# Kernel optimization log

Hardware: AMD Instinct MI355X
Metric: run time of the kernel (lower is better)

The kernel has to match this reference:

```python
import jax, jax.numpy as jnp
import numpy as np

N_NODES = 100000
N_EDGES = 1600000
IN_DIM = 128
HID_DIM = 128
N_MASK = 5000
N_CLASSES = 4


def gcn_layer(x, src, dst, edge_weight, W, b):
    """PyG GCNConv: x' = D^{-1/2} (A + I) D^{-1/2} (x W) + b, with edge weights."""
    n = x.shape[0]
    loop = jnp.arange(n, dtype=src.dtype)
    s = jnp.concatenate([src, loop])                      # [E+N]
    d = jnp.concatenate([dst, loop])                      # [E+N]
    w = jnp.concatenate([edge_weight, jnp.ones((n,), edge_weight.dtype)])
    deg = jax.ops.segment_sum(w, d, num_segments=n)       # weighted in-degree incl. self-loop
    dis = jnp.where(deg > 0, jax.lax.rsqrt(deg), 0.0)     # deg^{-1/2}, inf -> 0
    norm = dis[s] * w * dis[d]                            # [E+N]
    h = x @ W                                             # [N, H] small GEMM
    msg = h[s] * norm[:, None]                            # gather + scale  [E+N, H]
    out = jax.ops.segment_sum(msg, d, num_segments=n)     # scatter-add     [N, H]
    return out + b


def setup_inputs() -> dict:
    key = jax.random.key(0)
    ks = jax.random.split(key, 8)
    x = jax.random.normal(ks[0], (N_NODES, IN_DIM), dtype=jnp.float32)
    edge_weight = jax.random.uniform(ks[1], (N_EDGES,), dtype=jnp.float32)
    W1 = jax.random.normal(ks[2], (IN_DIM, HID_DIM), dtype=jnp.float32) * (1.0 / np.sqrt(IN_DIM))
    b1 = jnp.zeros((HID_DIM,), jnp.float32)
    W2 = jax.random.normal(ks[3], (HID_DIM, HID_DIM), dtype=jnp.float32) * (1.0 / np.sqrt(HID_DIM))
    b2 = jnp.zeros((HID_DIM,), jnp.float32)
    edge_index = jax.random.randint(ks[4], (2, N_EDGES), 0, N_NODES, dtype=jnp.int32)
    mask_idx = jax.random.randint(ks[5], (N_MASK,), 0, N_NODES, dtype=jnp.int32)
    y = jax.random.randint(ks[6], (N_NODES,), 0, N_CLASSES, dtype=jnp.int32)
    return {"x": x, "edge_weight": edge_weight, "W1": W1, "b1": b1,
            "W2": W2, "b2": b2, "edge_index": edge_index,
            "mask_idx": mask_idx, "y": y}


def reference(x, edge_weight, W1, b1, W2, b2, edge_index, mask_idx, y):
    src, dst = edge_index[0], edge_index[1]
    h = gcn_layer(x, src, dst, edge_weight, W1, b1)
    h = jax.nn.relu(h)
    # F.dropout(training=False) in eval mode is identity
    h = gcn_layer(h, src, dst, edge_weight, W2, b2)
    return h[mask_idx], y[mask_idx]
```

## Files before the change

kernel.cpp:

```cpp
#include <hip/hip_runtime.h>

constexpr int N = 100000;
constexpr int E = 1600000;
constexpr int D = 128;
constexpr int M = 5000;

constexpr int MF_BLKS = (N + 255) / 256;

constexpr int NB  = 196;
constexpr int EB  = 2048;
constexpr int NPB = (E + EB - 1) / EB;
constexpr int HL  = NB * NPB;
constexpr int SC_BLKS = (HL + 1023) / 1024;
constexpr int PREP_BLKS = 64;
constexpr int MB_BLKS = (M + 255) / 256;

typedef __attribute__((ext_vector_type(8))) short bf16x8;
typedef __attribute__((ext_vector_type(4))) float f32x4;


__device__ __forceinline__ unsigned int pack_bf16x2(float a, float b) {
    unsigned int ua = __float_as_uint(a);
    unsigned int ub = __float_as_uint(b);
    ua = (ua + 0x7FFFu + ((ua >> 16) & 1u)) >> 16;
    ub = (ub + 0x7FFFu + ((ub >> 16) & 1u)) & 0xFFFF0000u;
    return ua | ub;
}
__device__ __forceinline__ unsigned short bf16_rne(float a) {
    unsigned int ua = __float_as_uint(a);
    return (unsigned short)((ua + 0x7FFFu + ((ua >> 16) & 1u)) >> 16);
}
__device__ __forceinline__ float bf16_lo(unsigned int u) { return __uint_as_float(u << 16); }
__device__ __forceinline__ float bf16_hi(unsigned int u) { return __uint_as_float(u & 0xFFFF0000u); }


__global__ __launch_bounds__(256) void k_misc1(const int* __restrict__ dst,
                                               int* __restrict__ hist,
                                               const float* __restrict__ W1,
                                               unsigned int* __restrict__ Wt1,
                                               const float* __restrict__ W2,
                                               unsigned int* __restrict__ Wt2,
                                               const int* __restrict__ mask,
                                               unsigned int* __restrict__ maskbit,
                                               unsigned int* __restrict__ needed) {
    __shared__ int h[NB];
    const int t = threadIdx.x;
    if (blockIdx.x < NPB) {
        if (t < NB) h[t] = 0;
        __syncthreads();
        const int base = blockIdx.x * EB;
#pragma unroll
        for (int i = 0; i < 8; ++i) {
            int e = base + t + i * 256;
            if (e < E) {
                int b = __builtin_nontemporal_load(dst + e) >> 9;
                atomicAdd(&h[b], 1);
            }
        }
        __syncthreads();
        if (t < NB) hist[t * NPB + blockIdx.x] = h[t];
    } else if (blockIdx.x < NPB + PREP_BLKS) {
        int gi = (blockIdx.x - NPB) * 256 + t;
        const float* W = (gi < 8192) ? W1 : W2;
        unsigned int* Wt = (gi < 8192) ? Wt1 : Wt2;
        int idx = gi & 8191;
        int n = idx >> 6, kk = idx & 63;
        float a = W[(2 * kk) * D + n];
        float b = W[(2 * kk + 1) * D + n];
        Wt[idx] = pack_bf16x2(a, b);
    } else {
        int i = (blockIdx.x - NPB - PREP_BLKS) * 256 + t;
        if (i < M) {
            int n = mask[i];
            atomicOr(&maskbit[n >> 5], 1u << (n & 31));
            atomicOr(&needed[n >> 5], 1u << (n & 31));
        }
    }
}


__global__ __launch_bounds__(256) void k_misc2(const int* __restrict__ hist,
                                               int* __restrict__ bs,
                                               const unsigned int* __restrict__ maskbit,
                                               const int* __restrict__ src,
                                               const int* __restrict__ dst,
                                               unsigned int* __restrict__ needed) {
    __shared__ int ws_[4];
    const int t = threadIdx.x;
    if (blockIdx.x < SC_BLKS) {
        const int idx = blockIdx.x * 1024 + t * 4;
        int s = 0;
        if (idx + 3 < HL) {
            int4 c = *(const int4*)(hist + idx);
            s = c.x + c.y + c.z + c.w;
        } else {
            for (int i = 0; i < 4; ++i) if (idx + i < HL) s += hist[idx + i];
        }
        for (int off = 32; off > 0; off >>= 1) s += __shfl_down(s, off);
        if ((t & 63) == 0) ws_[t >> 6] = s;
        __syncthreads();
        if (t == 0) bs[blockIdx.x] = ws_[0] + ws_[1] + ws_[2] + ws_[3];
    } else {
        const int base = (blockIdx.x - SC_BLKS) * EB;
#pragma unroll
        for (int i = 0; i < 8; ++i) {
            int e = base + t + i * 256;
            if (e < E) {
                int d = __builtin_nontemporal_load(dst + e);
                if ((maskbit[d >> 5] >> (d & 31)) & 1u) {
                    int s = src[e];
                    atomicOr(&needed[s >> 5], 1u << (s & 31));
                }
            }
        }
    }
}


__global__ __launch_bounds__(256) void k_scanf(const int* __restrict__ hist,
                                               const int* __restrict__ bs,
                                               int* __restrict__ histS) {
    __shared__ int sh[256];
    __shared__ int waveS[4];
    const int t = threadIdx.x;
    const int lane = t & 63;
    const int wave = t >> 6;

    sh[t] = (t < SC_BLKS) ? bs[t] : 0;
    __syncthreads();
    for (int off = 1; off < 256; off <<= 1) {
        int u = (t >= off) ? sh[t - off] : 0;
        __syncthreads();
        sh[t] += u;
        __syncthreads();
    }
    const int bOff = sh[blockIdx.x] - bs[blockIdx.x];

    const int idx = blockIdx.x * 1024 + t * 4;
    int4 c = make_int4(0, 0, 0, 0);
    if (idx + 3 < HL) c = *(const int4*)(hist + idx);
    else {
        if (idx + 0 < HL) c.x = hist[idx + 0];
        if (idx + 1 < HL) c.y = hist[idx + 1];
        if (idx + 2 < HL) c.z = hist[idx + 2];
        if (idx + 3 < HL) c.w = hist[idx + 3];
    }
    int s = c.x + c.y + c.z + c.w;

    int v = s;
    for (int off = 1; off < 64; off <<= 1) {
        int u = __shfl_up(v, off);
        if (lane >= off) v += u;
    }
    if (lane == 63) waveS[wave] = v;
    __syncthreads();
    int waveBase = 0;
    for (int w = 0; w < 4; ++w) if (w < wave) waveBase += waveS[w];
    int excl = bOff + waveBase + (v - s);

    int4 rs;
    rs.x = excl;
    rs.y = excl + c.x;
    rs.z = excl + c.x + c.y;
    rs.w = excl + c.x + c.y + c.z;
    if (idx + 3 < HL) {
        *(int4*)(histS + idx) = rs;
    } else {
        if (idx + 0 < HL) histS[idx + 0] = rs.x;
        if (idx + 1 < HL) histS[idx + 1] = rs.y;
        if (idx + 2 < HL) histS[idx + 2] = rs.z;
        if (idx + 3 < HL) histS[idx + 3] = rs.w;
    }
}


template <bool BF16IN>
__device__ __forceinline__ void gemm_mfma_body(const void* __restrict__ Xin,
                                               const unsigned int* __restrict__ Wt,
                                               unsigned short* __restrict__ out, int blk) {
    __shared__ unsigned int Ws[128 * 68];
    const int t = threadIdx.x;
#pragma unroll
    for (int i = 0; i < 8; ++i) {
        int f4 = t + i * 256;
        int n = f4 >> 4;
        int k4 = f4 & 15;
        uint4 w = ((const uint4*)Wt)[f4];
        *(uint4*)(&Ws[n * 68 + k4 * 4]) = w;
    }
    __syncthreads();

    const int wv = t >> 6, lane = t & 63;
    const int q = lane >> 4, l15 = lane & 15;
    const int rowBase = blk * 256 + wv * 64;

    f32x4 acc[4][8] = {};
#pragma unroll
    for (int kc = 0; kc < 4; ++kc) {
        bf16x8 af[4];
#pragma unroll
        for (int rt = 0; rt < 4; ++rt) {
            int row = rowBase + rt * 16 + l15;
            if (row > N - 1) row = N - 1;
            union { uint4 u; bf16x8 v; } cv;
            if (BF16IN) {
                cv.u = *(const uint4*)((const unsigned int*)Xin + (size_t)row * 64 + kc * 16 + q * 4);
            } else {
                const float* xr = (const float*)Xin + (size_t)row * D + kc * 32 + q * 8;
                float4 x0 = *(const float4*)xr;
                float4 x1 = *(const float4*)(xr + 4);
                cv.u.x = pack_bf16x2(x0.x, x0.y);
                cv.u.y = pack_bf16x2(x0.z, x0.w);
                cv.u.z = pack_bf16x2(x1.x, x1.y);
                cv.u.w = pack_bf16x2(x1.z, x1.w);
            }
            af[rt] = cv.v;
        }
#pragma unroll
        for (int ct = 0; ct < 8; ++ct) {
            union { uint4 u; bf16x8 v; } bv;
            bv.u = *(const uint4*)(&Ws[(ct * 16 + l15) * 68 + kc * 16 + q * 4]);
#pragma unroll
            for (int rt = 0; rt < 4; ++rt)
                acc[rt][ct] = __builtin_amdgcn_mfma_f32_16x16x32_bf16(af[rt], bv.v, acc[rt][ct], 0, 0, 0);
        }
    }

#pragma unroll
    for (int rt = 0; rt < 4; ++rt) {
#pragma unroll
        for (int ct = 0; ct < 8; ++ct) {
            int col = ct * 16 + l15;
#pragma unroll
            for (int r = 0; r < 4; ++r) {
                int row = rowBase + rt * 16 + q * 4 + r;
                if (row < N) out[(size_t)row * D + col] = bf16_rne(acc[rt][ct][r]);
            }
        }
    }
}


__global__ __launch_bounds__(256) void k_part_g1(const int* __restrict__ src,
                                                 const int* __restrict__ dst,
                                                 const float* __restrict__ ew,
                                                 const int* __restrict__ histS,
                                                 unsigned long long* __restrict__ tmp,
                                                 const float* __restrict__ x,
                                                 const unsigned int* __restrict__ Wt1,
                                                 unsigned short* __restrict__ A) {
    if (blockIdx.x >= NPB) {
        gemm_mfma_body<false>(x, Wt1, A, blockIdx.x - NPB);
        return;
    }
    __shared__ int base_[NB];
    const int t = threadIdx.x;
    if (t < NB) base_[t] = histS[t * NPB + blockIdx.x];
    __syncthreads();
    const int eb = blockIdx.x * EB;
#pragma unroll
    for (int i = 0; i < 8; ++i) {
        int e = eb + t + i * 256;
        if (e < E) {
            int d = __builtin_nontemporal_load(dst + e);
            int s = __builtin_nontemporal_load(src + e);
            float w = __builtin_nontemporal_load(ew + e);
            int b = d >> 9;
            int pos = atomicAdd(&base_[b], 1);
            unsigned long long rec =
                ((unsigned long long)(unsigned int)__float_as_int(w) << 32) |
                ((unsigned int)s << 9) | (unsigned int)(d & 511);
            __builtin_nontemporal_store(rec, tmp + pos);
        }
    }
}

__global__ __launch_bounds__(256) void k_gemm2(const unsigned short* __restrict__ B,
                                               const unsigned int* __restrict__ Wt2,
                                               unsigned short* __restrict__ A2) {
    gemm_mfma_body<true>(B, Wt2, A2, blockIdx.x);
}


__global__ __launch_bounds__(256) void k_local(const unsigned long long* __restrict__ tmp,
                                               const int* __restrict__ histS,
                                               float* __restrict__ dis,
                                               int* __restrict__ rowStart,
                                               int2* __restrict__ pairs) {
    const int b = blockIdx.x;
    const int t = threadIdx.x;
    const int segBeg = histS[b * NPB];
    const int segEnd = (b + 1 < NB) ? histS[(b + 1) * NPB] : E;

    __shared__ int   cnt[512];
    __shared__ float wsum[512];
    __shared__ int   off[512];
    __shared__ int   waveS[4];
    cnt[t] = 0; cnt[t + 256] = 0;
    wsum[t] = 0.f; wsum[t + 256] = 0.f;
    __syncthreads();

    for (int e = segBeg + t; e < segEnd; e += 256) {
        unsigned long long rec = tmp[e];
        int dl = (int)(rec & 511);
        float w = __uint_as_float((unsigned int)(rec >> 32));
        atomicAdd(&cnt[dl], 1);
        atomicAdd(&wsum[dl], w);
    }
    __syncthreads();

    const int i0 = t * 2, i1 = t * 2 + 1;
    const int c0 = cnt[i0], c1 = cnt[i1];
    const int pv = c0 + c1;
    const int lane = t & 63, wv = t >> 6;
    int v = pv;
    for (int o = 1; o < 64; o <<= 1) {
        int u = __shfl_up(v, o);
        if (lane >= o) v += u;
    }
    if (lane == 63) waveS[wv] = v;
    __syncthreads();
    int wb = 0;
    for (int w = 0; w < 4; ++w) if (w < wv) wb += waveS[w];
    const int ex = wb + v - pv;
    off[i0] = ex;
    off[i1] = ex + c0;
    const int node0 = b * 512 + i0, node1 = b * 512 + i1;
    if (node0 < N) { rowStart[node0] = segBeg + ex;      dis[node0] = rsqrtf(1.0f + wsum[i0]); }
    if (node1 < N) { rowStart[node1] = segBeg + ex + c0; dis[node1] = rsqrtf(1.0f + wsum[i1]); }
    cnt[i0] = 0; cnt[i1] = 0;
    if (b == NB - 1 && t == 0) rowStart[N] = E;
    __syncthreads();

    for (int e = segBeg + t; e < segEnd; e += 256) {
        unsigned long long rec = tmp[e];
        int dl = (int)(rec & 511);
        int s  = (int)((rec >> 9) & 0xFFFFF);
        unsigned int wbits = (unsigned int)(rec >> 32);
        int r = atomicAdd(&cnt[dl], 1);
        pairs[segBeg + off[dl] + r] = make_int2(s, (int)wbits);
    }
}


__global__ __launch_bounds__(256) void k_aggregate(const unsigned int* __restrict__ Hb,
                                                   const int2* __restrict__ pairs,
                                                   const int* __restrict__ rowStart,
                                                   const float* __restrict__ dis,
                                                   const unsigned int* __restrict__ needed,
                                                   const float* __restrict__ b,
                                                   unsigned int* __restrict__ outB) {
    int node = blockIdx.x * 4 + (threadIdx.x >> 6);
    if (node >= N) return;
    if (!((needed[node >> 5] >> (node & 31)) & 1u)) return;
    int lane = threadIdx.x & 63;
    int beg = rowStart[node], end = rowStart[node + 1];

    float ax = 0.f, ay = 0.f;
    int j = beg;
    for (; j + 7 < end; j += 8) {
        int2 p[8];
        float vv[8];
        unsigned int h[8];
#pragma unroll
        for (int i = 0; i < 8; ++i) p[i] = pairs[j + i];
#pragma unroll
        for (int i = 0; i < 8; ++i) { h[i] = Hb[(size_t)p[i].x * 64 + lane]; vv[i] = dis[p[i].x]; }
#pragma unroll
        for (int i = 0; i < 8; ++i) {
            float v = __int_as_float(p[i].y) * vv[i];
            ax += bf16_lo(h[i]) * v;
            ay += bf16_hi(h[i]) * v;
        }
    }
    for (; j + 3 < end; j += 4) {
        int2 p[4];
        float vv[4];
        unsigned int h[4];
#pragma unroll
        for (int i = 0; i < 4; ++i) p[i] = pairs[j + i];
#pragma unroll
        for (int i = 0; i < 4; ++i) { h[i] = Hb[(size_t)p[i].x * 64 + lane]; vv[i] = dis[p[i].x]; }
#pragma unroll
        for (int i = 0; i < 4; ++i) {
            float v = __int_as_float(p[i].y) * vv[i];
            ax += bf16_lo(h[i]) * v;
            ay += bf16_hi(h[i]) * v;
        }
    }
    for (; j < end; ++j) {
        int2 p0 = pairs[j];
        unsigned int h0 = Hb[(size_t)p0.x * 64 + lane];
        float v0 = __int_as_float(p0.y) * dis[p0.x];
        ax += bf16_lo(h0) * v0;
        ay += bf16_hi(h0) * v0;
    }

    float dd = dis[node];
    float sn = dd * dd;
    unsigned int hs = Hb[(size_t)node * 64 + lane];
    float2 bb = ((const float2*)b)[lane];
    float ox = fmaxf(ax * dd + bf16_lo(hs) * sn + bb.x, 0.f);
    float oy = fmaxf(ay * dd + bf16_hi(hs) * sn + bb.y, 0.f);
    __builtin_nontemporal_store(pack_bf16x2(ox, oy), outB + (size_t)node * 64 + lane);
}


__global__ __launch_bounds__(256) void k_aggregate_mask(const unsigned int* __restrict__ Hb,
                                                        const int2* __restrict__ pairs,
                                                        const int* __restrict__ rowStart,
                                                        const float* __restrict__ dis,
                                                        const float* __restrict__ b,
                                                        const int* __restrict__ mask,
                                                        const int* __restrict__ y,
                                                        float* __restrict__ out) {
    int i = blockIdx.x * 4 + (threadIdx.x >> 6);
    if (i >= M) return;
    int lane = threadIdx.x & 63;
    int node = mask[i];
    int beg = rowStart[node], end = rowStart[node + 1];

    float ax = 0.f, ay = 0.f;
    int j = beg;
    for (; j + 7 < end; j += 8) {
        int2 p[8];
        float vv[8];
        unsigned int h[8];
#pragma unroll
        for (int ii = 0; ii < 8; ++ii) p[ii] = pairs[j + ii];
#pragma unroll
        for (int ii = 0; ii < 8; ++ii) { h[ii] = Hb[(size_t)p[ii].x * 64 + lane]; vv[ii] = dis[p[ii].x]; }
#pragma unroll
        for (int ii = 0; ii < 8; ++ii) {
            float v = __int_as_float(p[ii].y) * vv[ii];
            ax += bf16_lo(h[ii]) * v;
            ay += bf16_hi(h[ii]) * v;
        }
    }
    for (; j < end; ++j) {
        int2 p0 = pairs[j];
        unsigned int h0 = Hb[(size_t)p0.x * 64 + lane];
        float v0 = __int_as_float(p0.y) * dis[p0.x];
        ax += bf16_lo(h0) * v0;
        ay += bf16_hi(h0) * v0;
    }

    float dd = dis[node];
    float sn = dd * dd;
    unsigned int hs = Hb[(size_t)node * 64 + lane];
    float2 bb = ((const float2*)b)[lane];
    float ox = ax * dd + bf16_lo(hs) * sn + bb.x;
    float oy = ay * dd + bf16_hi(hs) * sn + bb.y;
    ((float2*)(out + (size_t)i * D))[lane] = make_float2(ox, oy);
    if (lane == 0) out[(size_t)M * D + i] = (float)y[node];
}

extern "C" void kernel_launch(void* const* d_in, const int* in_sizes, int n_in,
                              void* d_out, int out_size, void* d_ws, size_t ws_size,
                              hipStream_t stream) {
    const float* x  = (const float*)d_in[0];
    const float* ew = (const float*)d_in[1];
    const float* W1 = (const float*)d_in[2];
    const float* b1 = (const float*)d_in[3];
    const float* W2 = (const float*)d_in[4];
    const float* b2 = (const float*)d_in[5];
    const int* eidx = (const int*)d_in[6];
    const int* mask = (const int*)d_in[7];
    const int* y    = (const int*)d_in[8];
    const int* src = eidx;
    const int* dst = eidx + E;

    char* ws = (char*)d_ws;
    float* dis      = (float*)(ws);
    int*   rowStart = (int*)(ws + (size_t)512 * 1024);
    int*   scanBS   = (int*)(ws + (size_t)1024 * 1024);
    unsigned int* maskbit = (unsigned int*)(ws + (size_t)1056 * 1024);
    unsigned int* needed  = (unsigned int*)(ws + (size_t)1072 * 1024);
    unsigned int* Wt1 = (unsigned int*)(ws + (size_t)1088 * 1024);
    unsigned int* Wt2 = (unsigned int*)(ws + (size_t)1120 * 1024);
    int*   hist     = (int*)(ws + (size_t)1280 * 1024);
    int*   histS    = (int*)(ws + (size_t)1920 * 1024);
    int2*  pairs    = (int2*)(ws + (size_t)3 * 1024 * 1024);
    unsigned long long* tmp = (unsigned long long*)(ws + (size_t)16 * 1024 * 1024);
    unsigned short* A  = (unsigned short*)(ws + (size_t)29 * 1024 * 1024);
    unsigned short* B  = (unsigned short*)(ws + (size_t)55 * 1024 * 1024);
    unsigned short* A2 = (unsigned short*)(ws + (size_t)81 * 1024 * 1024);

    (void)hipMemsetAsync(maskbit, 0, (size_t)32 * 1024, stream);
    hipLaunchKernelGGL(k_misc1, dim3(NPB + PREP_BLKS + MB_BLKS), dim3(256), 0, stream,
                       dst, hist, W1, Wt1, W2, Wt2, mask, maskbit, needed);

    hipLaunchKernelGGL(k_misc2, dim3(SC_BLKS + NPB), dim3(256), 0, stream,
                       hist, scanBS, maskbit, src, dst, needed);
    hipLaunchKernelGGL(k_scanf, dim3(SC_BLKS), dim3(256), 0, stream, hist, scanBS, histS);

    hipLaunchKernelGGL(k_part_g1, dim3(NPB + MF_BLKS), dim3(256), 0, stream,
                       src, dst, ew, histS, tmp, x, Wt1, A);
    hipLaunchKernelGGL(k_local, dim3(NB), dim3(256), 0, stream, tmp, histS, dis, rowStart, pairs);

    hipLaunchKernelGGL(k_aggregate, dim3((N + 3) / 4), dim3(256), 0, stream,
                       (const unsigned int*)A, pairs, rowStart, dis, needed, b1,
                       (unsigned int*)B);

    hipLaunchKernelGGL(k_gemm2, dim3(MF_BLKS), dim3(256), 0, stream, B, Wt2, A2);
    hipLaunchKernelGGL(k_aggregate_mask, dim3((M + 3) / 4), dim3(256), 0, stream,
                       (const unsigned int*)A2, pairs, rowStart, dis, b2, mask, y, (float*)d_out);
}
```

Before: 290.0 us.

## Fuse CSR-build kernels into one cooperative kernel with grid syncs

```diff
diff --git a/kernel.cpp b/kernel.cpp
--- a/kernel.cpp
+++ b/kernel.cpp
@@ -1,4 +1,7 @@
 #include <hip/hip_runtime.h>
+#include <hip/hip_cooperative_groups.h>
+
+namespace cg = cooperative_groups;
 
 constexpr int N = 100000;
 constexpr int E = 1600000;
@@ -15,6 +18,13 @@
 constexpr int PREP_BLKS = 64;
 constexpr int MB_BLKS = (M + 255) / 256;
 
+constexpr int CSR_GRID = 768;
+constexpr int S0_UNITS = 2 + NPB + PREP_BLKS;
+constexpr int S1_UNITS = MB_BLKS + SC_BLKS;
+constexpr int S2_UNITS = NPB + SC_BLKS;
+constexpr int S3_UNITS = NPB;
+constexpr int S4_UNITS = NB;
+
 typedef __attribute__((ext_vector_type(8))) short bf16x8;
 typedef __attribute__((ext_vector_type(4))) float f32x4;
 
@@ -34,142 +44,231 @@
 __device__ __forceinline__ float bf16_hi(unsigned int u) { return __uint_as_float(u & 0xFFFF0000u); }
 
 
-__global__ __launch_bounds__(256) void k_misc1(const int* __restrict__ dst,
-                                               int* __restrict__ hist,
-                                               const float* __restrict__ W1,
-                                               unsigned int* __restrict__ Wt1,
-                                               const float* __restrict__ W2,
-                                               unsigned int* __restrict__ Wt2,
-                                               const int* __restrict__ mask,
-                                               unsigned int* __restrict__ maskbit,
-                                               unsigned int* __restrict__ needed) {
-    __shared__ int h[NB];
+__global__ __launch_bounds__(256) void k_csr(const int* __restrict__ src,
+                                             const int* __restrict__ dst,
+                                             const float* __restrict__ ew,
+                                             const int* __restrict__ mask,
+                                             const float* __restrict__ W1,
+                                             const float* __restrict__ W2,
+                                             int* __restrict__ hist,
+                                             int* __restrict__ bs,
+                                             int* __restrict__ histS,
+                                             unsigned long long* __restrict__ tmp,
+                                             int2* __restrict__ pairs,
+                                             float* __restrict__ dis,
+                                             int* __restrict__ rowStart,
+                                             unsigned int* __restrict__ maskbit,
+                                             unsigned int* __restrict__ needed,
+                                             unsigned int* __restrict__ Wt1,
+                                             unsigned int* __restrict__ Wt2) {
+    cg::grid_group grid = cg::this_grid();
     const int t = threadIdx.x;
-    if (blockIdx.x < NPB) {
-        if (t < NB) h[t] = 0;
-        __syncthreads();
-        const int base = blockIdx.x * EB;
+    const int nb = gridDim.x;
+
+    __shared__ int   h[NB];
+    __shared__ int   sh[256];
+    __shared__ int   waveS[4];
+    __shared__ int   cnt[512];
+    __shared__ float wsum[512];
+    __shared__ int   off[512];
+
+    for (int u = blockIdx.x; u < S0_UNITS; u += nb) {
+        if (u < 2) {
+            unsigned int* p = (u == 0) ? maskbit : needed;
+            for (int i = t; i < 4096; i += 256) p[i] = 0u;
+        } else if (u < 2 + NPB) {
+            const int ub = u - 2;
+            if (t < NB) h[t] = 0;
+            __syncthreads();
+            const int base = ub * EB;
+#pragma unroll
+            for (int i = 0; i < 8; ++i) {
+                int e = base + t + i * 256;
+                if (e < E) {
+                    int b = __builtin_nontemporal_load(dst + e) >> 9;
+                    atomicAdd(&h[b], 1);
+                }
+            }
+            __syncthreads();
+            if (t < NB) hist[t * NPB + ub] = h[t];
+            __syncthreads();
+        } else {
+            int gi = (u - 2 - NPB) * 256 + t;
+            const float* W = (gi < 8192) ? W1 : W2;
+            unsigned int* Wt = (gi < 8192) ? Wt1 : Wt2;
+            int idx = gi & 8191;
+            int n = idx >> 6, kk = idx & 63;
+            float a = W[(2 * kk) * D + n];
+            float b = W[(2 * kk + 1) * D + n];
+            Wt[idx] = pack_bf16x2(a, b);
+        }
+    }
+    grid.sync();
+
+    for (int u = blockIdx.x; u < S1_UNITS; u += nb) {
+        if (u < MB_BLKS) {
+            int i = u * 256 + t;
+            if (i < M) {
+                int n = mask[i];
+                atomicOr(&maskbit[n >> 5], 1u << (n & 31));
+                atomicOr(&needed[n >> 5], 1u << (n & 31));
+            }
+        } else {
+            const int ub = u - MB_BLKS;
+            const int idx = ub * 1024 + t * 4;
+            int s = 0;
+            if (idx + 3 < HL) {
+                int4 c = *(const int4*)(hist + idx);
+                s = c.x + c.y + c.z + c.w;
+            } else {
+                for (int i = 0; i < 4; ++i) if (idx + i < HL) s += hist[idx + i];
+            }
+            for (int o = 32; o > 0; o >>= 1) s += __shfl_down(s, o);
+            if ((t & 63) == 0) waveS[t >> 6] = s;
+            __syncthreads();
+            if (t == 0) bs[ub] = waveS[0] + waveS[1] + waveS[2] + waveS[3];
+            __syncthreads();
+        }
+    }
+    grid.sync();
+
+    for (int u = blockIdx.x; u < S2_UNITS; u += nb) {
+        if (u < NPB) {
+            const int base = u * EB;
+#pragma unroll
+            for (int i = 0; i < 8; ++i) {
+                int e = base + t + i * 256;
+                if (e < E) {
+                    int d = __builtin_nontemporal_load(dst + e);
+                    if ((maskbit[d >> 5] >> (d & 31)) & 1u) {
+                        int s = src[e];
+                        atomicOr(&needed[s >> 5], 1u << (s & 31));
+                    }
+                }
+            }
+        } else {
+            const int ub = u - NPB;
+            sh[t] = (t < SC_BLKS) ? bs[t] : 0;
+            __syncthreads();
+            for (int o = 1; o < 256; o <<= 1) {
+                int v2 = (t >= o) ? sh[t - o] : 0;
+                __syncthreads();
+                sh[t] += v2;
+                __syncthreads();
+            }
+            const int bOff = sh[ub] - bs[ub];
+
+            const int idx = ub * 1024 + t * 4;
+            int4 c = make_int4(0, 0, 0, 0);
+            if (idx + 3 < HL) c = *(const int4*)(hist + idx);
+            else {
+                if (idx + 0 < HL) c.x = hist[idx + 0];
+                if (idx + 1 < HL) c.y = hist[idx + 1];
+                if (idx + 2 < HL) c.z = hist[idx + 2];
+                if (idx + 3 < HL) c.w = hist[idx + 3];
+            }
+            int s = c.x + c.y + c.z + c.w;
+            const int lane = t & 63, wv = t >> 6;
+            int v = s;
+            for (int o = 1; o < 64; o <<= 1) {
+                int u2 = __shfl_up(v, o);
+                if (lane >= o) v += u2;
+            }
+            if (lane == 63) waveS[wv] = v;
+            __syncthreads();
+            int wb = 0;
+            for (int w = 0; w < 4; ++w) if (w < wv) wb += waveS[w];
+            int excl = bOff + wb + (v - s);
+
+            int4 rs;
+            rs.x = excl;
+            rs.y = excl + c.x;
+            rs.z = excl + c.x + c.y;
+            rs.w = excl + c.x + c.y + c.z;
+            if (idx + 3 < HL) *(int4*)(histS + idx) = rs;
+            else {
+                if (idx + 0 < HL) histS[idx + 0] = rs.x;
+                if (idx + 1 < HL) histS[idx + 1] = rs.y;
+                if (idx + 2 < HL) histS[idx + 2] = rs.z;
+                if (idx + 3 < HL) histS[idx + 3] = rs.w;
+            }
+            __syncthreads();
+        }
+    }
+    grid.sync();
+
+    for (int u = blockIdx.x; u < S3_UNITS; u += nb) {
+        if (t < NB) h[t] = histS[t * NPB + u];
+        __syncthreads();
+        const int eb = u * EB;
 #pragma unroll
         for (int i = 0; i < 8; ++i) {
-            int e = base + t + i * 256;
-            if (e < E) {
-                int b = __builtin_nontemporal_load(dst + e) >> 9;
-                atomicAdd(&h[b], 1);
-            }
-        }
-        __syncthreads();
-        if (t < NB) hist[t * NPB + blockIdx.x] = h[t];
-    } else if (blockIdx.x < NPB + PREP_BLKS) {
-        int gi = (blockIdx.x - NPB) * 256 + t;
-        const float* W = (gi < 8192) ? W1 : W2;
-        unsigned int* Wt = (gi < 8192) ? Wt1 : Wt2;
-        int idx = gi & 8191;
-        int n = idx >> 6, kk = idx & 63;
-        float a = W[(2 * kk) * D + n];
-        float b = W[(2 * kk + 1) * D + n];
-        Wt[idx] = pack_bf16x2(a, b);
-    } else {
-        int i = (blockIdx.x - NPB - PREP_BLKS) * 256 + t;
-        if (i < M) {
-            int n = mask[i];
-            atomicOr(&maskbit[n >> 5], 1u << (n & 31));
-            atomicOr(&needed[n >> 5], 1u << (n & 31));
-        }
-    }
-}
-
-
-__global__ __launch_bounds__(256) void k_misc2(const int* __restrict__ hist,
-                                               int* __restrict__ bs,
-                                               const unsigned int* __restrict__ maskbit,
-                                               const int* __restrict__ src,
-                                               const int* __restrict__ dst,
-                                               unsigned int* __restrict__ needed) {
-    __shared__ int ws_[4];
-    const int t = threadIdx.x;
-    if (blockIdx.x < SC_BLKS) {
-        const int idx = blockIdx.x * 1024 + t * 4;
-        int s = 0;
-        if (idx + 3 < HL) {
-            int4 c = *(const int4*)(hist + idx);
-            s = c.x + c.y + c.z + c.w;
-        } else {
-            for (int i = 0; i < 4; ++i) if (idx + i < HL) s += hist[idx + i];
-        }
-        for (int off = 32; off > 0; off >>= 1) s += __shfl_down(s, off);
-        if ((t & 63) == 0) ws_[t >> 6] = s;
-        __syncthreads();
-        if (t == 0) bs[blockIdx.x] = ws_[0] + ws_[1] + ws_[2] + ws_[3];
-    } else {
-        const int base = (blockIdx.x - SC_BLKS) * EB;
-#pragma unroll
-        for (int i = 0; i < 8; ++i) {
-            int e = base + t + i * 256;
+            int e = eb + t + i * 256;
             if (e < E) {
                 int d = __builtin_nontemporal_load(dst + e);
-                if ((maskbit[d >> 5] >> (d & 31)) & 1u) {
-                    int s = src[e];
-                    atomicOr(&needed[s >> 5], 1u << (s & 31));
-                }
-            }
-        }
-    }
-}
-
-
-__global__ __launch_bounds__(256) void k_scanf(const int* __restrict__ hist,
-                                               const int* __restrict__ bs,
-                                               int* __restrict__ histS) {
-    __shared__ int sh[256];
-    __shared__ int waveS[4];
-    const int t = threadIdx.x;
-    const int lane = t & 63;
-    const int wave = t >> 6;
-
-    sh[t] = (t < SC_BLKS) ? bs[t] : 0;
-    __syncthreads();
-    for (int off = 1; off < 256; off <<= 1) {
-        int u = (t >= off) ? sh[t - off] : 0;
-        __syncthreads();
-        sh[t] += u;
-        __syncthreads();
-    }
-    const int bOff = sh[blockIdx.x] - bs[blockIdx.x];
-
-    const int idx = blockIdx.x * 1024 + t * 4;
-    int4 c = make_int4(0, 0, 0, 0);
-    if (idx + 3 < HL) c = *(const int4*)(hist + idx);
-    else {
-        if (idx + 0 < HL) c.x = hist[idx + 0];
-        if (idx + 1 < HL) c.y = hist[idx + 1];
-        if (idx + 2 < HL) c.z = hist[idx + 2];
-        if (idx + 3 < HL) c.w = hist[idx + 3];
-    }
-    int s = c.x + c.y + c.z + c.w;
-
-    int v = s;
-    for (int off = 1; off < 64; off <<= 1) {
-        int u = __shfl_up(v, off);
-        if (lane >= off) v += u;
-    }
-    if (lane == 63) waveS[wave] = v;
-    __syncthreads();
-    int waveBase = 0;
-    for (int w = 0; w < 4; ++w) if (w < wave) waveBase += waveS[w];
-    int excl = bOff + waveBase + (v - s);
-
-    int4 rs;
-    rs.x = excl;
-    rs.y = excl + c.x;
-    rs.z = excl + c.x + c.y;
-    rs.w = excl + c.x + c.y + c.z;
-    if (idx + 3 < HL) {
-        *(int4*)(histS + idx) = rs;
-    } else {
-        if (idx + 0 < HL) histS[idx + 0] = rs.x;
-        if (idx + 1 < HL) histS[idx + 1] = rs.y;
-        if (idx + 2 < HL) histS[idx + 2] = rs.z;
-        if (idx + 3 < HL) histS[idx + 3] = rs.w;
+                int s = __builtin_nontemporal_load(src + e);
+                float w = __builtin_nontemporal_load(ew + e);
+                int b = d >> 9;
+                int pos = atomicAdd(&h[b], 1);
+                unsigned long long rec =
+                    ((unsigned long long)(unsigned int)__float_as_int(w) << 32) |
+                    ((unsigned int)s << 9) | (unsigned int)(d & 511);
+                __builtin_nontemporal_store(rec, tmp + pos);
+            }
+        }
+        __syncthreads();
+    }
+    grid.sync();
+
+    for (int u = blockIdx.x; u < S4_UNITS; u += nb) {
+        const int segBeg = histS[u * NPB];
+        const int segEnd = (u + 1 < NB) ? histS[(u + 1) * NPB] : E;
+
+        cnt[t] = 0; cnt[t + 256] = 0;
+        wsum[t] = 0.f; wsum[t + 256] = 0.f;
+        __syncthreads();
+
+        for (int e = segBeg + t; e < segEnd; e += 256) {
+            unsigned long long rec = tmp[e];
+            int dl = (int)(rec & 511);
+            float w = __uint_as_float((unsigned int)(rec >> 32));
+            atomicAdd(&cnt[dl], 1);
+            atomicAdd(&wsum[dl], w);
+        }
+        __syncthreads();
+
+        const int i0 = t * 2, i1 = t * 2 + 1;
+        const int c0 = cnt[i0], c1 = cnt[i1];
+        const int pv = c0 + c1;
+        const int lane = t & 63, wv = t >> 6;
+        int v = pv;
+        for (int o = 1; o < 64; o <<= 1) {
+            int u2 = __shfl_up(v, o);
+            if (lane >= o) v += u2;
+        }
+        if (lane == 63) waveS[wv] = v;
+        __syncthreads();
+        int wb = 0;
+        for (int w = 0; w < 4; ++w) if (w < wv) wb += waveS[w];
+        const int ex = wb + v - pv;
+        off[i0] = ex;
+        off[i1] = ex + c0;
+        const int node0 = u * 512 + i0, node1 = u * 512 + i1;
+        if (node0 < N) { rowStart[node0] = segBeg + ex;      dis[node0] = rsqrtf(1.0f + wsum[i0]); }
+        if (node1 < N) { rowStart[node1] = segBeg + ex + c0; dis[node1] = rsqrtf(1.0f + wsum[i1]); }
+        cnt[i0] = 0; cnt[i1] = 0;
+        if (u == NB - 1 && t == 0) rowStart[N] = E;
+        __syncthreads();
+
+        for (int e = segBeg + t; e < segEnd; e += 256) {
+            unsigned long long rec = tmp[e];
+            int dl = (int)(rec & 511);
+            int s  = (int)((rec >> 9) & 0xFFFFF);
+            unsigned int wbits = (unsigned int)(rec >> 32);
+            int r = atomicAdd(&cnt[dl], 1);
+            pairs[segBeg + off[dl] + r] = make_int2(s, (int)wbits);
+        }
+        __syncthreads();
     }
 }
 
@@ -240,106 +339,16 @@
     }
 }
 
-
-__global__ __launch_bounds__(256) void k_part_g1(const int* __restrict__ src,
-                                                 const int* __restrict__ dst,
-                                                 const float* __restrict__ ew,
-                                                 const int* __restrict__ histS,
-                                                 unsigned long long* __restrict__ tmp,
-                                                 const float* __restrict__ x,
-                                                 const unsigned int* __restrict__ Wt1,
-                                                 unsigned short* __restrict__ A) {
-    if (blockIdx.x >= NPB) {
-        gemm_mfma_body<false>(x, Wt1, A, blockIdx.x - NPB);
-        return;
-    }
-    __shared__ int base_[NB];
-    const int t = threadIdx.x;
-    if (t < NB) base_[t] = histS[t * NPB + blockIdx.x];
-    __syncthreads();
-    const int eb = blockIdx.x * EB;
-#pragma unroll
-    for (int i = 0; i < 8; ++i) {
-        int e = eb + t + i * 256;
-        if (e < E) {
-            int d = __builtin_nontemporal_load(dst + e);
-            int s = __builtin_nontemporal_load(src + e);
-            float w = __builtin_nontemporal_load(ew + e);
-            int b = d >> 9;
-            int pos = atomicAdd(&base_[b], 1);
-            unsigned long long rec =
-                ((unsigned long long)(unsigned int)__float_as_int(w) << 32) |
-                ((unsigned int)s << 9) | (unsigned int)(d & 511);
-            __builtin_nontemporal_store(rec, tmp + pos);
-        }
-    }
+__global__ __launch_bounds__(256) void k_gemm1(const float* __restrict__ x,
+                                               const unsigned int* __restrict__ Wt1,
+                                               unsigned short* __restrict__ A) {
+    gemm_mfma_body<false>(x, Wt1, A, blockIdx.x);
 }
 
 __global__ __launch_bounds__(256) void k_gemm2(const unsigned short* __restrict__ B,
                                                const unsigned int* __restrict__ Wt2,
                                                unsigned short* __restrict__ A2) {
     gemm_mfma_body<true>(B, Wt2, A2, blockIdx.x);
-}
-
-
-__global__ __launch_bounds__(256) void k_local(const unsigned long long* __restrict__ tmp,
-                                               const int* __restrict__ histS,
-                                               float* __restrict__ dis,
-                                               int* __restrict__ rowStart,
-                                               int2* __restrict__ pairs) {
-    const int b = blockIdx.x;
-    const int t = threadIdx.x;
-    const int segBeg = histS[b * NPB];
-    const int segEnd = (b + 1 < NB) ? histS[(b + 1) * NPB] : E;
-
-    __shared__ int   cnt[512];
-    __shared__ float wsum[512];
-    __shared__ int   off[512];
-    __shared__ int   waveS[4];
-    cnt[t] = 0; cnt[t + 256] = 0;
-    wsum[t] = 0.f; wsum[t + 256] = 0.f;
-    __syncthreads();
-
-    for (int e = segBeg + t; e < segEnd; e += 256) {
-        unsigned long long rec = tmp[e];
-        int dl = (int)(rec & 511);
-        float w = __uint_as_float((unsigned int)(rec >> 32));
-        atomicAdd(&cnt[dl], 1);
-        atomicAdd(&wsum[dl], w);
-    }
-    __syncthreads();
-
-    const int i0 = t * 2, i1 = t * 2 + 1;
-    const int c0 = cnt[i0], c1 = cnt[i1];
-    const int pv = c0 + c1;
-    const int lane = t & 63, wv = t >> 6;
-    int v = pv;
-    for (int o = 1; o < 64; o <<= 1) {
-        int u = __shfl_up(v, o);
-        if (lane >= o) v += u;
-    }
-    if (lane == 63) waveS[wv] = v;
-    __syncthreads();
-    int wb = 0;
-    for (int w = 0; w < 4; ++w) if (w < wv) wb += waveS[w];
-    const int ex = wb + v - pv;
-    off[i0] = ex;
-    off[i1] = ex + c0;
-    const int node0 = b * 512 + i0, node1 = b * 512 + i1;
-    if (node0 < N) { rowStart[node0] = segBeg + ex;      dis[node0] = rsqrtf(1.0f + wsum[i0]); }
-    if (node1 < N) { rowStart[node1] = segBeg + ex + c0; dis[node1] = rsqrtf(1.0f + wsum[i1]); }
-    cnt[i0] = 0; cnt[i1] = 0;
-    if (b == NB - 1 && t == 0) rowStart[N] = E;
-    __syncthreads();
-
-    for (int e = segBeg + t; e < segEnd; e += 256) {
-        unsigned long long rec = tmp[e];
-        int dl = (int)(rec & 511);
-        int s  = (int)((rec >> 9) & 0xFFFFF);
-        unsigned int wbits = (unsigned int)(rec >> 32);
-        int r = atomicAdd(&cnt[dl], 1);
-        pairs[segBeg + off[dl] + r] = make_int2(s, (int)wbits);
-    }
 }
 
 
@@ -486,18 +495,16 @@
     unsigned short* B  = (unsigned short*)(ws + (size_t)55 * 1024 * 1024);
     unsigned short* A2 = (unsigned short*)(ws + (size_t)81 * 1024 * 1024);
 
-    (void)hipMemsetAsync(maskbit, 0, (size_t)32 * 1024, stream);
-    hipLaunchKernelGGL(k_misc1, dim3(NPB + PREP_BLKS + MB_BLKS), dim3(256), 0, stream,
-                       dst, hist, W1, Wt1, W2, Wt2, mask, maskbit, needed);
-
-    hipLaunchKernelGGL(k_misc2, dim3(SC_BLKS + NPB), dim3(256), 0, stream,
-                       hist, scanBS, maskbit, src, dst, needed);
-    hipLaunchKernelGGL(k_scanf, dim3(SC_BLKS), dim3(256), 0, stream, hist, scanBS, histS);
-
-    hipLaunchKernelGGL(k_part_g1, dim3(NPB + MF_BLKS), dim3(256), 0, stream,
-                       src, dst, ew, histS, tmp, x, Wt1, A);
-    hipLaunchKernelGGL(k_local, dim3(NB), dim3(256), 0, stream, tmp, histS, dis, rowStart, pairs);
-
+    void* csrArgs[] = {
+        (void*)&src, (void*)&dst, (void*)&ew, (void*)&mask, (void*)&W1, (void*)&W2,
+        (void*)&hist, (void*)&scanBS, (void*)&histS, (void*)&tmp, (void*)&pairs,
+        (void*)&dis, (void*)&rowStart, (void*)&maskbit, (void*)&needed,
+        (void*)&Wt1, (void*)&Wt2,
+    };
+    (void)hipLaunchCooperativeKernel((const void*)k_csr, dim3(CSR_GRID), dim3(256),
+                                     csrArgs, 0, stream);
+
+    hipLaunchKernelGGL(k_gemm1, dim3(MF_BLKS), dim3(256), 0, stream, x, Wt1, A);
     hipLaunchKernelGGL(k_aggregate, dim3((N + 3) / 4), dim3(256), 0, stream,
                        (const unsigned int*)A, pairs, rowStart, dis, needed, b1,
                        (unsigned int*)B);
```

Result: slower. 670.3 us (+131.1%).
